# Kernel optimization log

Measured on AMD Instinct MI355X. Metric: run time of the kernel, lower is better.

Reference implementation:

```python
import jax, jax.numpy as jnp
import numpy as np

D = 128
N = 20000
E = 60000
L = 5  # levels 0..4; level 0 = primary inputs
PER = N // L
# processing order in the original forward: AND(3), NOT(2), XOR(5), MAJ(1), OR(4)
CODES = [3, 2, 5, 1, 4]
FIDX = {3: 0, 5: 1, 1: 2, 4: 3}  # index into 2D-input func aggregators


def _gru(x, h, wih, whh, bih, bhh):
    # single-step torch.nn.GRU cell. wih:[D,3D], whh:[D,3D]
    gi = x @ wih + bih
    gh = h @ whh + bhh
    ir, iz, inn = jnp.split(gi, 3, axis=-1)
    hr, hz, hn = jnp.split(gh, 3, axis=-1)
    r = jax.nn.sigmoid(ir + hr)
    z = jax.nn.sigmoid(iz + hz)
    n = jnp.tanh(inn + r * hn)
    return (1.0 - z) * n + z * h


def setup_inputs() -> dict:
    rng = np.random.default_rng(0)
    # topological levels, contiguous blocks of PER nodes per level
    forward_level = np.repeat(np.arange(L), PER).astype(np.int32)
    gate = np.zeros(N, dtype=np.int32)
    gate[PER:] = rng.integers(1, 6, size=N - PER)  # gates 1..5 for non-PI nodes
    # DAG edges: dst at level>=1, src strictly below dst's level
    dst = rng.integers(PER, N, size=E)
    dst_level = forward_level[dst].astype(np.int64)
    src = (rng.random(E) * (dst_level * PER)).astype(np.int64)
    edge_index = np.stack([src, dst]).astype(np.int32)

    key = jax.random.key(0)
    ks = iter(jax.random.split(key, 64))
    s = 0.08
    p = {}
    p['hs_init'] = jax.random.normal(next(ks), (N, D), jnp.float32)
    # strc aggregators (5 gate types, input D): 2-layer MLP
    p['Ws1'] = jax.random.normal(next(ks), (5, D, D)) * s
    p['bs1'] = jnp.zeros((5, D))
    p['Ws2'] = jax.random.normal(next(ks), (5, D, D)) * s
    p['bs2'] = jnp.zeros((5, D))
    # func aggregators with 2D input (and, xor, maj, or)
    p['Wf1'] = jax.random.normal(next(ks), (4, 2 * D, D)) * s
    p['bf1'] = jnp.zeros((4, D))
    p['Wf2'] = jax.random.normal(next(ks), (4, D, D)) * s
    p['bf2'] = jnp.zeros((4, D))
    # not_func aggregator (input D)
    p['Wnf1'] = jax.random.normal(next(ks), (D, D)) * s
    p['bnf1'] = jnp.zeros((D,))
    p['Wnf2'] = jax.random.normal(next(ks), (D, D)) * s
    p['bnf2'] = jnp.zeros((D,))
    # GRU params, stacked over 5 gate types, strc and func
    for pre in ('Gs', 'Gf'):
        p[pre + '_wih'] = jax.random.normal(next(ks), (5, D, 3 * D)) * s
        p[pre + '_whh'] = jax.random.normal(next(ks), (5, D, 3 * D)) * s
        p[pre + '_bih'] = jnp.zeros((5, 3 * D))
        p[pre + '_bhh'] = jnp.zeros((5, 3 * D))
    p['edge_index'] = jnp.asarray(edge_index)
    p['gate'] = jnp.asarray(gate)
    p['forward_level'] = jnp.asarray(forward_level)
    p['num_levels'] = L
    return p


def reference(hs_init, Ws1, bs1, Ws2, bs2, Wf1, bf1, Wf2, bf2,
              Wnf1, bnf1, Wnf2, bnf2,
              Gs_wih, Gs_whh, Gs_bih, Gs_bhh,
              Gf_wih, Gf_whh, Gf_bih, Gf_bhh,
              edge_index, gate, forward_level, num_levels):
    src, dst = edge_index[0], edge_index[1]
    pi_mask = (gate == 0)
    hs = jnp.where(pi_mask[:, None], hs_init, 0.0)  # generate_hs_init: encode PIs
    hf = jnp.zeros_like(hs)
    node_state = jnp.concatenate([hs, hf], axis=-1)

    for level in range(1, num_levels):
        for t, code in enumerate(CODES):
            nmask = (forward_level == level) & (gate == code)  # [N]
            emask = nmask[dst].astype(hs.dtype)[:, None]       # edges into these nodes
            # --- structural message: MLP(hs[src]) summed into dst
            m = jax.nn.relu(hs[src] @ Ws1[t] + bs1[t]) @ Ws2[t] + bs2[t]
            agg = jax.ops.segment_sum(m * emask, dst, num_segments=N)
            h_new = _gru(agg, hs, Gs_wih[t], Gs_whh[t], Gs_bih[t], Gs_bhh[t])
            hs = jnp.where(nmask[:, None], h_new, hs)
            # --- functional message
            if code == 2:  # NOT uses current hf only
                m = jax.nn.relu(hf[src] @ Wnf1 + bnf1) @ Wnf2 + bnf2
            else:
                fi = FIDX[code]
                m = jax.nn.relu(node_state[src] @ Wf1[fi] + bf1[fi]) @ Wf2[fi] + bf2[fi]
            agg = jax.ops.segment_sum(m * emask, dst, num_segments=N)
            h_new = _gru(agg, hf, Gf_wih[t], Gf_whh[t], Gf_bih[t], Gf_bhh[t])
            hf = jnp.where(nmask[:, None], h_new, hf)
        node_state = jnp.concatenate([hs, hf], axis=-1)
    return hs, hf
```

## Files before the change

kernel.cpp:

```cpp
#include <hip/hip_runtime.h>
#include <hip/hip_bf16.h>

typedef __hip_bfloat16 bf16;
typedef unsigned short ushortT;
typedef __attribute__((ext_vector_type(8))) short bf16x8;
typedef __attribute__((ext_vector_type(4))) float f32x4;

#define D 128
#define NLEV 5
#define TE 16
#define TN 16

#define OFF_S1 0
#define OFF_S2 81920
#define OFF_F1 163840
#define OFF_F2 294912
#define OFF_NF1 360448
#define OFF_NF2 376832
#define OFF_GSH 393216
#define OFF_GFH 638976
#define OFF_GSL 884736
#define OFF_GFL 1130496
#define WT_TOTAL 1376256

__constant__ int TMAP[6] = { -1, 3, 1, 0, 4, 2 };
__constant__ int FMAP[6] = { -1, 2, -1, 0, 3, 1 };

__device__ int g_flag;

__device__ __forceinline__ float sigm(float x) { return 1.0f / (1.0f + __expf(-x)); }

__device__ __forceinline__ ushortT f2b(float v) {
    bf16 h = __float2bfloat16(v);
    return *reinterpret_cast<ushortT*>(&h);
}

template <int ISB>
__device__ __forceinline__ float ld(const void* p, size_t i) {
    if (ISB) return __bfloat162float(((const bf16*)p)[i]);
    return ((const float*)p)[i];
}

__device__ __forceinline__ float ldx(int isb, const void* p, size_t i) {
    return isb ? __bfloat162float(((const bf16*)p)[i]) : ((const float*)p)[i];
}

__global__ __launch_bounds__(256) void setup_a(
    const void* __restrict__ hs_init, const int* __restrict__ gate,
    const int* __restrict__ dstA, const int* __restrict__ lev,
    int E, int N, int ND,
    ushortT* __restrict__ hsb, ushortT* __restrict__ hfb, void* __restrict__ out,
    float* __restrict__ agg_s, float* __restrict__ agg_f,
    int* __restrict__ ecnt, int* __restrict__ ncnt, int* __restrict__ ndeg,
    const void* Ws1, const void* Ws2, const void* Wf1, const void* Wf2,
    const void* Wnf1, const void* Wnf2, const void* Gs, const void* Gf,
    ushortT* __restrict__ wt, int B_init, int B_cnt) {
    __shared__ int sfl;
    __shared__ int lc[40];
    int tid = threadIdx.x;
    int bid = blockIdx.x;

    if (tid < 64) {
        float x = __bfloat162float(((const bf16*)hs_init)[2 * tid]);
        float ax = fabsf(x);
        bool sane = (x == 0.0f) || (ax > 1e-4f && ax < 64.0f);
        unsigned long long m = __ballot(sane);
        if (tid == 0) sfl = (__popcll(m) >= 32) ? 1 : 0;
    }
    __syncthreads();
    int isb = sfl;
    if (bid == 0 && tid == 0) g_flag = isb;

    if (bid < B_init) {
        int v = (bid << 1) | (tid >> 7);
        int j = tid & 127;
        if (v < N) {
            size_t idx = (size_t)v * D + j;
            bool pi = (gate[v] == 0);
            if (isb) {
                ushortT bval = pi ? ((const ushortT*)hs_init)[idx] : 0;
                hsb[idx] = bval; hfb[idx] = 0;
                ((ushortT*)out)[idx] = bval;
                ((ushortT*)out)[ND + idx] = 0;
            } else {
                float val = pi ? ((const float*)hs_init)[idx] : 0.f;
                hsb[idx] = f2b(val); hfb[idx] = 0;
                ((float*)out)[idx] = val;
                ((float*)out)[ND + idx] = 0.f;
            }
            agg_s[idx] = 0.f;
            agg_f[idx] = 0.f;
        }
    } else if (bid < B_init + B_cnt) {
        if (tid < 40) lc[tid] = 0;
        __syncthreads();
        int i = (bid - B_init) * 256 + tid;
        if (i < E) {
            int d = dstA[i]; int l = lev[d];
            if (l >= 1 && l < NLEV) {
                atomicAdd(&lc[(l - 1) * 5 + TMAP[gate[d]]], 1);
                atomicAdd(&ndeg[d], 1);
            }
        }
        if (i < N) {
            int l = lev[i];
            if (l >= 1 && l < NLEV && gate[i] >= 1)
                atomicAdd(&lc[20 + (l - 1) * 5 + TMAP[gate[i]]], 1);
        }
        __syncthreads();
        if (tid < 20 && lc[tid]) atomicAdd(&ecnt[tid], lc[tid]);
        if (tid >= 20 && tid < 40 && lc[tid]) atomicAdd(&ncnt[tid - 20], lc[tid]);
    } else {
        int i = (bid - B_init - B_cnt) * 256 + tid;
        if (i >= WT_TOTAL) return;
        const void* src; int Kd, C, rem, mode = 0;
        if (i < OFF_S2)       { src = Ws1;  rem = i;           Kd = 128; C = 128; }
        else if (i < OFF_F1)  { src = Ws2;  rem = i - OFF_S2;  Kd = 128; C = 128; }
        else if (i < OFF_F2)  { src = Wf1;  rem = i - OFF_F1;  Kd = 256; C = 128; }
        else if (i < OFF_NF1) { src = Wf2;  rem = i - OFF_F2;  Kd = 128; C = 128; }
        else if (i < OFF_NF2) { src = Wnf1; rem = i - OFF_NF1; Kd = 128; C = 128; }
        else if (i < OFF_GSH) { src = Wnf2; rem = i - OFF_NF2; Kd = 128; C = 128; }
        else if (i < OFF_GFH) { src = Gs;   rem = i - OFF_GSH; Kd = 128; C = 384; mode = 1; }
        else if (i < OFF_GSL) { src = Gf;   rem = i - OFF_GFH; Kd = 128; C = 384; mode = 1; }
        else if (i < OFF_GFL) { src = Gs;   rem = i - OFF_GSL; Kd = 128; C = 384; mode = 2; }
        else                  { src = Gf;   rem = i - OFF_GFL; Kd = 128; C = 384; mode = 2; }
        int n = rem / (Kd * C);
        int r2 = rem % (Kd * C);
        int c = r2 / Kd;
        int k = r2 % Kd;
        size_t si = (size_t)n * Kd * C + (size_t)k * C + c;
        float v = ldx(isb, src, si);
        ushortT o;
        if (mode == 2) {
            bf16 h = __float2bfloat16(v);
            o = f2b(v - __bfloat162float(h));
        } else {
            o = f2b(v);
        }
        wt[i] = o;
    }
}

__global__ void scan_offsets(const int* __restrict__ ecnt, const int* __restrict__ ncnt,
                             int* __restrict__ eoff, int* __restrict__ noff) {
    if (threadIdx.x == 0 && blockIdx.x == 0) {
        int o = 0;
        for (int b = 0; b < 20; ++b) { eoff[b] = o; o += ((ecnt[b] + TE - 1) / TE) * TE; }
        eoff[20] = o;
        o = 0;
        for (int b = 0; b < 20; ++b) { noff[b] = o; o += ((ncnt[b] + TN - 1) / TN) * TN; }
        noff[20] = o;
    }
}

__global__ void fill_bins(const int* __restrict__ gate, const int* __restrict__ lev, int N,
                          const int* __restrict__ noff, int* __restrict__ ncur,
                          int* __restrict__ nlist) {
    __shared__ int nc[20], nb[20];
    int tid = threadIdx.x;
    if (tid < 20) nc[tid] = 0;
    __syncthreads();
    int i = blockIdx.x * blockDim.x + tid;
    int bn = -1, rn = 0;
    if (i < N) {
        int l = lev[i];
        if (l >= 1 && l < NLEV && gate[i] >= 1) { bn = (l - 1) * 5 + TMAP[gate[i]]; rn = atomicAdd(&nc[bn], 1); }
    }
    __syncthreads();
    if (tid < 20) nb[tid] = nc[tid] ? atomicAdd(&ncur[tid], nc[tid]) : 0;
    __syncthreads();
    if (bn >= 0) nlist[noff[bn] + nb[bn] + rn] = i;
}

__global__ __launch_bounds__(256) void bucket_scan(
    const int* __restrict__ nlist, const int* __restrict__ noff,
    const int* __restrict__ ncnt, const int* __restrict__ eoff,
    const int* __restrict__ ndeg, int* __restrict__ nodeoff) {
    int b = blockIdx.x;
    int start = noff[b];
    int cnt = ncnt[b];
    int ebase = eoff[b];
    __shared__ int sc[256];
    int tid = threadIdx.x;
    int carry = 0;
    for (int chunk = 0; chunk < cnt; chunk += 256) {
        __syncthreads();
        int i = chunk + tid;
        int v = -1, dg = 0;
        if (i < cnt) { v = nlist[start + i]; dg = ndeg[v]; }
        sc[tid] = dg;
        __syncthreads();
        for (int off = 1; off < 256; off <<= 1) {
            int y = (tid >= off) ? sc[tid - off] : 0;
            __syncthreads();
            sc[tid] += y;
            __syncthreads();
        }
        if (v >= 0) nodeoff[v] = ebase + carry + (sc[tid] - dg);
        carry += sc[255];
    }
}

__global__ void fill_edges(const int* __restrict__ dstA, const int* __restrict__ lev,
                           int E, const int* __restrict__ nodeoff,
                           int* __restrict__ ecur_n, int* __restrict__ elist) {
    int i = blockIdx.x * blockDim.x + threadIdx.x;
    if (i >= E) return;
    int d = dstA[i];
    int l = lev[d];
    if (l >= 1 && l < NLEV) {
        int pos = nodeoff[d] + atomicAdd(&ecur_n[d], 1);
        elist[pos] = i;
    }
}

__global__ __launch_bounds__(256) void edge_mfma(
    const ushortT* __restrict__ hsb, const ushortT* __restrict__ hfb,
    const ushortT* __restrict__ wt,
    const void* __restrict__ bs1, const void* __restrict__ bs2,
    const void* __restrict__ bf1, const void* __restrict__ bf2,
    const void* __restrict__ bnf1, const void* __restrict__ bnf2,
    const int* __restrict__ dstA, const int* __restrict__ srcA,
    const int* __restrict__ gate,
    const int* __restrict__ eoff, const int* __restrict__ ecnt,
    const int* __restrict__ elist,
    float* __restrict__ agg_s, float* __restrict__ agg_f, int level) {
    int lvl = (level - 1) * 5;
    int lo = eoff[lvl];
    int hi = eoff[lvl + 5];
    int base = lo + blockIdx.x * TE;
    if (base >= hi) return;
    int b = 0;
#pragma unroll
    for (int bb = 1; bb < 5; ++bb) if (base >= eoff[lvl + bb]) b = bb;
    int nvalid = eoff[lvl + b] + ecnt[lvl + b] - base;
    if (nvalid <= 0) return;
    if (nvalid > TE) nvalid = TE;

    __shared__ int se[TE], de[TE];
    __shared__ bf16 hid[2][16][136];
    __shared__ float emsg[2][16][128];

    int tid = threadIdx.x;
    int wv = tid >> 6, pass = wv >> 1, hc = wv & 1, l = tid & 63;
    int lg = l >> 4, lr = l & 15;
    int isb = g_flag;

    int c = gate[dstA[elist[base]]];
    int t = TMAP[c], fi = FMAP[c];

    if (tid < TE) {
        if (tid < nvalid) {
            int e = elist[base + tid];
            se[tid] = srcA[e];
            de[tid] = dstA[e];
        } else {
            se[tid] = -1;
            de[tid] = -1;
        }
    }
    __syncthreads();

    int src = se[lr];

    int KS1; size_t wb1; int K1;
    if (pass == 0)      { KS1 = 4; wb1 = OFF_S1 + (size_t)t * 16384; K1 = 128; }
    else if (c == 2)    { KS1 = 4; wb1 = OFF_NF1; K1 = 128; }
    else                { KS1 = 8; wb1 = OFF_F1 + (size_t)fi * 32768; K1 = 256; }

    f32x4 a0 = {0.f,0.f,0.f,0.f}, a1 = a0, a2 = a0, a3 = a0;
    for (int ks = 0; ks < KS1; ++ks) {
        bf16x8 a = {0,0,0,0,0,0,0,0};
        if (src >= 0) {
            int kk = ks * 32 + lg * 8;
            const ushortT* ap;
            if (pass == 0)      ap = hsb + (size_t)src * D + kk;
            else if (c == 2)    ap = hfb + (size_t)src * D + kk;
            else                ap = (kk < 128) ? (hsb + (size_t)src * D + kk)
                                                : (hfb + (size_t)src * D + (kk - 128));
            a = *(const bf16x8*)ap;
        }
        int kb = ks * 32 + lg * 8;
        {
            bf16x8 b2 = *(const bf16x8*)&wt[wb1 + (size_t)(hc * 64 + 0 * 16 + lr) * K1 + kb];
            a0 = __builtin_amdgcn_mfma_f32_16x16x32_bf16(a, b2, a0, 0, 0, 0);
        }
        {
            bf16x8 b2 = *(const bf16x8*)&wt[wb1 + (size_t)(hc * 64 + 1 * 16 + lr) * K1 + kb];
            a1 = __builtin_amdgcn_mfma_f32_16x16x32_bf16(a, b2, a1, 0, 0, 0);
        }
        {
            bf16x8 b2 = *(const bf16x8*)&wt[wb1 + (size_t)(hc * 64 + 2 * 16 + lr) * K1 + kb];
            a2 = __builtin_amdgcn_mfma_f32_16x16x32_bf16(a, b2, a2, 0, 0, 0);
        }
        {
            bf16x8 b2 = *(const bf16x8*)&wt[wb1 + (size_t)(hc * 64 + 3 * 16 + lr) * K1 + kb];
            a3 = __builtin_amdgcn_mfma_f32_16x16x32_bf16(a, b2, a3, 0, 0, 0);
        }
    }

    const void* b1p = (pass == 0) ? bs1 : (c == 2 ? bnf1 : bf1);
    size_t b1o = (pass == 0) ? (size_t)t * D : (c == 2 ? 0 : (size_t)fi * D);
    {
        f32x4 av[4] = { a0, a1, a2, a3 };
#pragma unroll
        for (int ct = 0; ct < 4; ++ct) {
            int cc = hc * 64 + ct * 16 + lr;
            float bb = ldx(isb, b1p, b1o + cc);
#pragma unroll
            for (int r = 0; r < 4; ++r) {
                int m = lg * 4 + r;
                float v = fmaxf(av[ct][r] + bb, 0.f);
                hid[pass][m][cc] = __float2bfloat16(v);
            }
        }
    }
    __syncthreads();

    size_t wb2 = (pass == 0) ? (OFF_S2 + (size_t)t * 16384)
                             : (c == 2 ? (size_t)OFF_NF2 : (OFF_F2 + (size_t)fi * 16384));
    a0 = (f32x4){0.f,0.f,0.f,0.f}; a1 = a0; a2 = a0; a3 = a0;
#pragma unroll
    for (int ks = 0; ks < 4; ++ks) {
        bf16x8 a = *(const bf16x8*)&hid[pass][lr][ks * 32 + lg * 8];
        int kb = ks * 32 + lg * 8;
        {
            bf16x8 b2 = *(const bf16x8*)&wt[wb2 + (size_t)(hc * 64 + 0 * 16 + lr) * 128 + kb];
            a0 = __builtin_amdgcn_mfma_f32_16x16x32_bf16(a, b2, a0, 0, 0, 0);
        }
        {
            bf16x8 b2 = *(const bf16x8*)&wt[wb2 + (size_t)(hc * 64 + 1 * 16 + lr) * 128 + kb];
            a1 = __builtin_amdgcn_mfma_f32_16x16x32_bf16(a, b2, a1, 0, 0, 0);
        }
        {
            bf16x8 b2 = *(const bf16x8*)&wt[wb2 + (size_t)(hc * 64 + 2 * 16 + lr) * 128 + kb];
            a2 = __builtin_amdgcn_mfma_f32_16x16x32_bf16(a, b2, a2, 0, 0, 0);
        }
        {
            bf16x8 b2 = *(const bf16x8*)&wt[wb2 + (size_t)(hc * 64 + 3 * 16 + lr) * 128 + kb];
            a3 = __builtin_amdgcn_mfma_f32_16x16x32_bf16(a, b2, a3, 0, 0, 0);
        }
    }

    const void* b2p = (pass == 0) ? bs2 : (c == 2 ? bnf2 : bf2);
    size_t b2o = (pass == 0) ? (size_t)t * D : (c == 2 ? 0 : (size_t)fi * D);
    {
        f32x4 av[4] = { a0, a1, a2, a3 };
#pragma unroll
        for (int ct = 0; ct < 4; ++ct) {
            int cc = hc * 64 + ct * 16 + lr;
            float bb = ldx(isb, b2p, b2o + cc);
#pragma unroll
            for (int r = 0; r < 4; ++r) {
                int m = lg * 4 + r;
                emsg[pass][m][cc] = av[ct][r] + bb;
            }
        }
    }
    __syncthreads();

    float* aggp = pass ? agg_f : agg_s;
    int col = hc * 64 + l;
    float s = 0.f;
    for (int m = 0; m < TE; ++m) {
        int d = de[m];
        if (d < 0) break;
        s += emsg[pass][m][col];
        bool flush = (m == TE - 1) || (de[m + 1] != d);
        if (flush) {
            atomicAdd(&aggp[(size_t)d * D + col], s);
            s = 0.f;
        }
    }
}

template <int ISB>
__device__ void node_fused_body(
    const float* __restrict__ agg_s, const float* __restrict__ agg_f,
    const ushortT* __restrict__ wt,
    const void* __restrict__ Gs_bih, const void* __restrict__ Gs_bhh,
    const void* __restrict__ Gf_bih, const void* __restrict__ Gf_bhh,
    ushortT* __restrict__ hsb, ushortT* __restrict__ hfb,
    void* __restrict__ out, int ND,
    const int* __restrict__ gate,
    const int* __restrict__ noff, const int* __restrict__ ncnt,
    const int* __restrict__ nlist,
    int level, float (*gi)[3][16][128]) {
    int lvl = (level - 1) * 5;
    int lo = noff[lvl];
    int hi = noff[lvl + 5];
    int base = lo + blockIdx.x * TN;
    if (base >= hi) return;
    int b = 0;
#pragma unroll
    for (int bb = 1; bb < 5; ++bb) if (base >= noff[lvl + bb]) b = bb;
    int nvalid = noff[lvl + b] + ncnt[lvl + b] - base;
    if (nvalid <= 0) return;
    if (nvalid > TN) nvalid = TN;

    int tid = threadIdx.x;
    int w = tid >> 6, l = tid & 63;
    int lg = l >> 4, lr = l & 15;
    int p = w / 6, cg = w % 6;
    int t = TMAP[gate[nlist[base]]];

    const float* agg = p ? agg_f : agg_s;
    size_t wbh = (p ? OFF_GFH : OFF_GSH) + (size_t)t * 49152;
    size_t wbl = (p ? OFF_GFL : OFF_GSL) + (size_t)t * 49152;

    int v = (lr < nvalid) ? nlist[base + lr] : -1;

    f32x4 acc[4];
#pragma unroll
    for (int q = 0; q < 4; ++q) acc[q] = (f32x4){0.f, 0.f, 0.f, 0.f};

    for (int ks = 0; ks < 4; ++ks) {
        bf16x8 ahi = {0,0,0,0,0,0,0,0}, alo = ahi;
        if (v >= 0) {
            const float* ap = agg + (size_t)v * D + ks * 32 + lg * 8;
            float4 f0 = *(const float4*)ap;
            float4 f1 = *(const float4*)(ap + 4);
            float av[8] = { f0.x, f0.y, f0.z, f0.w, f1.x, f1.y, f1.z, f1.w };
#pragma unroll
            for (int j = 0; j < 8; ++j) {
                bf16 h = __float2bfloat16(av[j]);
                ahi[j] = (short)*reinterpret_cast<ushortT*>(&h);
                float r = av[j] - __bfloat162float(h);
                bf16 l2 = __float2bfloat16(r);
                alo[j] = (short)*reinterpret_cast<ushortT*>(&l2);
            }
        }
        int kb = ks * 32 + lg * 8;
#pragma unroll
        for (int q = 0; q < 4; ++q) {
            int col = (cg * 4 + q) * 16 + lr;
            bf16x8 bh = *(const bf16x8*)&wt[wbh + (size_t)col * 128 + kb];
            acc[q] = __builtin_amdgcn_mfma_f32_16x16x32_bf16(ahi, bh, acc[q], 0, 0, 0);
            acc[q] = __builtin_amdgcn_mfma_f32_16x16x32_bf16(alo, bh, acc[q], 0, 0, 0);
            if (!ISB) {
                bf16x8 bl = *(const bf16x8*)&wt[wbl + (size_t)col * 128 + kb];
                acc[q] = __builtin_amdgcn_mfma_f32_16x16x32_bf16(ahi, bl, acc[q], 0, 0, 0);
            }
        }
    }

#pragma unroll
    for (int q = 0; q < 4; ++q) {
        int ct = cg * 4 + q;
        int g = ct >> 3, j = (ct & 7) * 16 + lr;
#pragma unroll
        for (int r = 0; r < 4; ++r) gi[p][g][lg * 4 + r][j] = acc[q][r];
    }
    __syncthreads();

    if (tid < 256) {
        int pp = tid >> 7, j = tid & 127;
        const void* bih = pp ? Gf_bih : Gs_bih;
        const void* bhh = pp ? Gf_bhh : Gs_bhh;
        float br = ld<ISB>(bih, (size_t)t * 384 + j);
        float bz = ld<ISB>(bih, (size_t)t * 384 + 128 + j);
        float bn = ld<ISB>(bih, (size_t)t * 384 + 256 + j);
        float hr = ld<ISB>(bhh, (size_t)t * 384 + j);
        float hz = ld<ISB>(bhh, (size_t)t * 384 + 128 + j);
        float hn = ld<ISB>(bhh, (size_t)t * 384 + 256 + j);
        ushortT* hb = pp ? hfb : hsb;
#pragma unroll
        for (int r = 0; r < TN; ++r) {
            if (r >= nvalid) break;
            int vv = nlist[base + r];
            float rr = sigm(gi[pp][0][r][j] + br + hr);
            float z = sigm(gi[pp][1][r][j] + bz + hz);
            float n = tanhf(gi[pp][2][r][j] + bn + rr * hn);
            float outv = (1.f - z) * n;
            size_t oidx = (size_t)pp * ND + (size_t)vv * D + j;
            if (ISB) ((ushortT*)out)[oidx] = f2b(outv);
            else     ((float*)out)[oidx] = outv;
            hb[(size_t)vv * D + j] = f2b(outv);
        }
    }
}

__global__ __launch_bounds__(768) void node_fused(
    const float* agg_s, const float* agg_f, const ushortT* wt,
    const void* Gs_bih, const void* Gs_bhh,
    const void* Gf_bih, const void* Gf_bhh,
    ushortT* hsb, ushortT* hfb, void* out, int ND,
    const int* gate, const int* noff, const int* ncnt, const int* nlist, int level) {
    __shared__ float gi[2][3][16][128];
    if (g_flag)
        node_fused_body<1>(agg_s, agg_f, wt, Gs_bih, Gs_bhh, Gf_bih, Gf_bhh,
                           hsb, hfb, out, ND, gate, noff, ncnt, nlist, level, gi);
    else
        node_fused_body<0>(agg_s, agg_f, wt, Gs_bih, Gs_bhh, Gf_bih, Gf_bhh,
                           hsb, hfb, out, ND, gate, noff, ncnt, nlist, level, gi);
}

extern "C" void kernel_launch(void* const* d_in, const int* in_sizes, int n_in,
                              void* d_out, int out_size, void* d_ws, size_t ws_size,
                              hipStream_t stream) {
    const void* hs_init = d_in[0];
    const void* Ws1 = d_in[1];
    const void* bs1 = d_in[2];
    const void* Ws2 = d_in[3];
    const void* bs2 = d_in[4];
    const void* Wf1 = d_in[5];
    const void* bf1 = d_in[6];
    const void* Wf2 = d_in[7];
    const void* bf2 = d_in[8];
    const void* Wnf1 = d_in[9];
    const void* bnf1 = d_in[10];
    const void* Wnf2 = d_in[11];
    const void* bnf2 = d_in[12];
    const void* Gs_wih = d_in[13];
    const void* Gs_bih = d_in[15];
    const void* Gs_bhh = d_in[16];
    const void* Gf_wih = d_in[17];
    const void* Gf_bih = d_in[19];
    const void* Gf_bhh = d_in[20];
    const int* edge_index = (const int*)d_in[21];
    const int* gate = (const int*)d_in[22];
    const int* lev = (const int*)d_in[23];

    int E = in_sizes[21] / 2;
    int N = in_sizes[22];
    int ND = N * D;
    int cap = ((N / NLEV + 5 * TN + 64) + TN - 1) / TN * TN;

    float* agg_s = (float*)d_ws;
    float* agg_f = agg_s + ND;
    ushortT* hsb = (ushortT*)(agg_f + ND);
    ushortT* hfb = hsb + ND;
    ushortT* wt = hfb + ND;
    int* meta = (int*)(wt + WT_TOTAL);
    int* ecnt = meta;
    int* ncnt = ecnt + 20;
    int* ncur = ncnt + 20;
    int* eoff = ncur + 20;
    int* noff = eoff + 21;
    int* ndeg = meta + 128;
    int* ecur_n = ndeg + N;
    int* nodeoff = ecur_n + N;
    int* elist = nodeoff + N;
    int* nlist = elist + (E + 20 * TE);

    const int* srcA = edge_index;
    const int* dstA = edge_index + E;

    hipMemsetAsync(meta, 0, (size_t)(128 + 2 * N) * sizeof(int), stream);

    int mx = (E > N) ? E : N;
    int B_init = (N + 1) / 2;
    int B_cnt = (mx + 255) / 256;
    int B_prep = (WT_TOTAL + 255) / 256;
    setup_a<<<B_init + B_cnt + B_prep, 256, 0, stream>>>(
        hs_init, gate, dstA, lev, E, N, ND,
        hsb, hfb, d_out, agg_s, agg_f,
        ecnt, ncnt, ndeg,
        Ws1, Ws2, Wf1, Wf2, Wnf1, Wnf2, Gs_wih, Gf_wih,
        wt, B_init, B_cnt);

    scan_offsets<<<1, 64, 0, stream>>>(ecnt, ncnt, eoff, noff);
    fill_bins<<<(N + 255) / 256, 256, 0, stream>>>(gate, lev, N, noff, ncur, nlist);
    bucket_scan<<<20, 256, 0, stream>>>(nlist, noff, ncnt, eoff, ndeg, nodeoff);
    fill_edges<<<(E + 255) / 256, 256, 0, stream>>>(dstA, lev, E, nodeoff, ecur_n, elist);

    int gridE = (E + 20 * TE) / TE + 1;
    int gridNcap = cap / TN;
    for (int level = 1; level < NLEV; ++level) {
        edge_mfma<<<gridE, 256, 0, stream>>>(hsb, hfb, wt,
                                             bs1, bs2, bf1, bf2, bnf1, bnf2,
                                             dstA, srcA, gate, eoff, ecnt, elist,
                                             agg_s, agg_f, level);
        node_fused<<<gridNcap, 768, 0, stream>>>(agg_s, agg_f, wt,
                                                 Gs_bih, Gs_bhh, Gf_bih, Gf_bhh,
                                                 hsb, hfb, d_out, ND,
                                                 gate, noff, ncnt, nlist, level);
    }
}
```

Before: 242.1 us.

## Merge setup kernels, vectorize init, and make edge kernel grid-stride persistent

Folds the single-thread offset scan into every fill_bins block and merges fill_edges into the bucket scan kernel, which now has each of 20 blocks scan all edges for its own bucket. This cuts two kernel launches. The init path now writes 4 elements per thread with vector stores. edge_mfma changes from one launch-sized grid to a fixed 2048-block grid-stride loop to cut block launch overhead and reuse LDS, at the cost of extra block-level syncs per tile and 20x redundant edge reads in finish_buckets.

```diff
diff --git a/kernel.cpp b/kernel.cpp
--- a/kernel.cpp
+++ b/kernel.cpp
@@ -3,6 +3,7 @@
 
 typedef __hip_bfloat16 bf16;
 typedef unsigned short ushortT;
+typedef unsigned int uintT;
 typedef __attribute__((ext_vector_type(8))) short bf16x8;
 typedef __attribute__((ext_vector_type(4))) float f32x4;
 
@@ -10,6 +11,7 @@
 #define NLEV 5
 #define TE 16
 #define TN 16
+#define EGRID 2048
 
 #define OFF_S1 0
 #define OFF_S2 81920
@@ -72,24 +74,30 @@
     if (bid == 0 && tid == 0) g_flag = isb;
 
     if (bid < B_init) {
-        int v = (bid << 1) | (tid >> 7);
-        int j = tid & 127;
+        int v = (bid << 3) | (tid >> 5);
+        int j = (tid & 31) * 4;
         if (v < N) {
             size_t idx = (size_t)v * D + j;
             bool pi = (gate[v] == 0);
             if (isb) {
-                ushortT bval = pi ? ((const ushortT*)hs_init)[idx] : 0;
-                hsb[idx] = bval; hfb[idx] = 0;
-                ((ushortT*)out)[idx] = bval;
-                ((ushortT*)out)[ND + idx] = 0;
+                uint2 bv = make_uint2(0u, 0u);
+                if (pi) bv = *(const uint2*)((const ushortT*)hs_init + idx);
+                *(uint2*)&hsb[idx] = bv;
+                *(uint2*)&hfb[idx] = make_uint2(0u, 0u);
+                *(uint2*)&((ushortT*)out)[idx] = bv;
+                *(uint2*)&((ushortT*)out)[ND + idx] = make_uint2(0u, 0u);
             } else {
-                float val = pi ? ((const float*)hs_init)[idx] : 0.f;
-                hsb[idx] = f2b(val); hfb[idx] = 0;
-                ((float*)out)[idx] = val;
-                ((float*)out)[ND + idx] = 0.f;
-            }
-            agg_s[idx] = 0.f;
-            agg_f[idx] = 0.f;
+                float4 fv = make_float4(0.f, 0.f, 0.f, 0.f);
+                if (pi) fv = *(const float4*)((const float*)hs_init + idx);
+                ushortT b0 = f2b(fv.x), b1 = f2b(fv.y), b2 = f2b(fv.z), b3 = f2b(fv.w);
+                *(uint2*)&hsb[idx] = make_uint2((uintT)b0 | ((uintT)b1 << 16),
+                                                (uintT)b2 | ((uintT)b3 << 16));
+                *(uint2*)&hfb[idx] = make_uint2(0u, 0u);
+                *(float4*)&((float*)out)[idx] = fv;
+                *(float4*)&((float*)out)[ND + idx] = make_float4(0.f, 0.f, 0.f, 0.f);
+            }
+            *(float4*)&agg_s[idx] = make_float4(0.f, 0.f, 0.f, 0.f);
+            *(float4*)&agg_f[idx] = make_float4(0.f, 0.f, 0.f, 0.f);
         }
     } else if (bid < B_init + B_cnt) {
         if (tid < 40) lc[tid] = 0;
@@ -141,25 +149,27 @@
     }
 }
 
-__global__ void scan_offsets(const int* __restrict__ ecnt, const int* __restrict__ ncnt,
-                             int* __restrict__ eoff, int* __restrict__ noff) {
-    if (threadIdx.x == 0 && blockIdx.x == 0) {
-        int o = 0;
-        for (int b = 0; b < 20; ++b) { eoff[b] = o; o += ((ecnt[b] + TE - 1) / TE) * TE; }
-        eoff[20] = o;
-        o = 0;
-        for (int b = 0; b < 20; ++b) { noff[b] = o; o += ((ncnt[b] + TN - 1) / TN) * TN; }
-        noff[20] = o;
-    }
-}
-
 __global__ void fill_bins(const int* __restrict__ gate, const int* __restrict__ lev, int N,
-                          const int* __restrict__ noff, int* __restrict__ ncur,
-                          int* __restrict__ nlist) {
+                          const int* __restrict__ ecnt, const int* __restrict__ ncnt,
+                          int* __restrict__ eoff, int* __restrict__ noff,
+                          int* __restrict__ ncur, int* __restrict__ nlist) {
+    __shared__ int s_noff[21], s_eoff[21];
     __shared__ int nc[20], nb[20];
     int tid = threadIdx.x;
+    if (tid == 0) {
+        int o = 0;
+        for (int b = 0; b < 20; ++b) { s_noff[b] = o; o += ((ncnt[b] + TN - 1) / TN) * TN; }
+        s_noff[20] = o;
+        o = 0;
+        for (int b = 0; b < 20; ++b) { s_eoff[b] = o; o += ((ecnt[b] + TE - 1) / TE) * TE; }
+        s_eoff[20] = o;
+    }
     if (tid < 20) nc[tid] = 0;
     __syncthreads();
+    if (blockIdx.x == 0 && tid < 21) {
+        noff[tid] = s_noff[tid];
+        eoff[tid] = s_eoff[tid];
+    }
     int i = blockIdx.x * blockDim.x + tid;
     int bn = -1, rn = 0;
     if (i < N) {
@@ -169,13 +179,16 @@
     __syncthreads();
     if (tid < 20) nb[tid] = nc[tid] ? atomicAdd(&ncur[tid], nc[tid]) : 0;
     __syncthreads();
-    if (bn >= 0) nlist[noff[bn] + nb[bn] + rn] = i;
-}
-
-__global__ __launch_bounds__(256) void bucket_scan(
+    if (bn >= 0) nlist[s_noff[bn] + nb[bn] + rn] = i;
+}
+
+__global__ __launch_bounds__(256) void finish_buckets(
     const int* __restrict__ nlist, const int* __restrict__ noff,
     const int* __restrict__ ncnt, const int* __restrict__ eoff,
-    const int* __restrict__ ndeg, int* __restrict__ nodeoff) {
+    const int* __restrict__ ndeg, int* __restrict__ nodeoff,
+    const int* __restrict__ dstA, const int* __restrict__ lev,
+    const int* __restrict__ gate, int E,
+    int* __restrict__ ecur_n, int* __restrict__ elist) {
     int b = blockIdx.x;
     int start = noff[b];
     int cnt = ncnt[b];
@@ -199,16 +212,13 @@
         if (v >= 0) nodeoff[v] = ebase + carry + (sc[tid] - dg);
         carry += sc[255];
     }
-}
-
-__global__ void fill_edges(const int* __restrict__ dstA, const int* __restrict__ lev,
-                           int E, const int* __restrict__ nodeoff,
-                           int* __restrict__ ecur_n, int* __restrict__ elist) {
-    int i = blockIdx.x * blockDim.x + threadIdx.x;
-    if (i >= E) return;
-    int d = dstA[i];
-    int l = lev[d];
-    if (l >= 1 && l < NLEV) {
+    __threadfence_block();
+    __syncthreads();
+    int blev = b / 5 + 1, bt = b % 5;
+    for (int i = tid; i < E; i += 256) {
+        int d = dstA[i];
+        if (lev[d] != blev) continue;
+        if (TMAP[gate[d]] != bt) continue;
         int pos = nodeoff[d] + atomicAdd(&ecur_n[d], 1);
         elist[pos] = i;
     }
@@ -227,15 +237,7 @@
     float* __restrict__ agg_s, float* __restrict__ agg_f, int level) {
     int lvl = (level - 1) * 5;
     int lo = eoff[lvl];
-    int hi = eoff[lvl + 5];
-    int base = lo + blockIdx.x * TE;
-    if (base >= hi) return;
-    int b = 0;
-#pragma unroll
-    for (int bb = 1; bb < 5; ++bb) if (base >= eoff[lvl + bb]) b = bb;
-    int nvalid = eoff[lvl + b] + ecnt[lvl + b] - base;
-    if (nvalid <= 0) return;
-    if (nvalid > TE) nvalid = TE;
+    int nt = (eoff[lvl + 5] - lo) / TE;
 
     __shared__ int se[TE], de[TE];
     __shared__ bf16 hid[2][16][136];
@@ -246,131 +248,142 @@
     int lg = l >> 4, lr = l & 15;
     int isb = g_flag;
 
-    int c = gate[dstA[elist[base]]];
-    int t = TMAP[c], fi = FMAP[c];
-
-    if (tid < TE) {
-        if (tid < nvalid) {
-            int e = elist[base + tid];
-            se[tid] = srcA[e];
-            de[tid] = dstA[e];
-        } else {
-            se[tid] = -1;
-            de[tid] = -1;
-        }
-    }
-    __syncthreads();
-
-    int src = se[lr];
-
-    int KS1; size_t wb1; int K1;
-    if (pass == 0)      { KS1 = 4; wb1 = OFF_S1 + (size_t)t * 16384; K1 = 128; }
-    else if (c == 2)    { KS1 = 4; wb1 = OFF_NF1; K1 = 128; }
-    else                { KS1 = 8; wb1 = OFF_F1 + (size_t)fi * 32768; K1 = 256; }
-
-    f32x4 a0 = {0.f,0.f,0.f,0.f}, a1 = a0, a2 = a0, a3 = a0;
-    for (int ks = 0; ks < KS1; ++ks) {
-        bf16x8 a = {0,0,0,0,0,0,0,0};
-        if (src >= 0) {
-            int kk = ks * 32 + lg * 8;
-            const ushortT* ap;
-            if (pass == 0)      ap = hsb + (size_t)src * D + kk;
-            else if (c == 2)    ap = hfb + (size_t)src * D + kk;
-            else                ap = (kk < 128) ? (hsb + (size_t)src * D + kk)
-                                                : (hfb + (size_t)src * D + (kk - 128));
-            a = *(const bf16x8*)ap;
-        }
-        int kb = ks * 32 + lg * 8;
+    for (int ti = blockIdx.x; ti < nt; ti += gridDim.x) {
+        int base = lo + ti * TE;
+        int b = 0;
+#pragma unroll
+        for (int bb = 1; bb < 5; ++bb) if (base >= eoff[lvl + bb]) b = bb;
+        int nvalid = eoff[lvl + b] + ecnt[lvl + b] - base;
+        if (nvalid <= 0) continue;
+        if (nvalid > TE) nvalid = TE;
+
+        int c = gate[dstA[elist[base]]];
+        int t = TMAP[c], fi = FMAP[c];
+
+        if (tid < TE) {
+            if (tid < nvalid) {
+                int e = elist[base + tid];
+                se[tid] = srcA[e];
+                de[tid] = dstA[e];
+            } else {
+                se[tid] = -1;
+                de[tid] = -1;
+            }
+        }
+        __syncthreads();
+
+        int src = se[lr];
+
+        int KS1; size_t wb1; int K1;
+        if (pass == 0)      { KS1 = 4; wb1 = OFF_S1 + (size_t)t * 16384; K1 = 128; }
+        else if (c == 2)    { KS1 = 4; wb1 = OFF_NF1; K1 = 128; }
+        else                { KS1 = 8; wb1 = OFF_F1 + (size_t)fi * 32768; K1 = 256; }
+
+        f32x4 a0 = {0.f,0.f,0.f,0.f}, a1 = a0, a2 = a0, a3 = a0;
+        for (int ks = 0; ks < KS1; ++ks) {
+            bf16x8 a = {0,0,0,0,0,0,0,0};
+            if (src >= 0) {
+                int kk = ks * 32 + lg * 8;
+                const ushortT* ap;
+                if (pass == 0)      ap = hsb + (size_t)src * D + kk;
+                else if (c == 2)    ap = hfb + (size_t)src * D + kk;
+                else                ap = (kk < 128) ? (hsb + (size_t)src * D + kk)
+                                                    : (hfb + (size_t)src * D + (kk - 128));
+                a = *(const bf16x8*)ap;
+            }
+            int kb = ks * 32 + lg * 8;
+            {
+                bf16x8 b2 = *(const bf16x8*)&wt[wb1 + (size_t)(hc * 64 + 0 * 16 + lr) * K1 + kb];
+                a0 = __builtin_amdgcn_mfma_f32_16x16x32_bf16(a, b2, a0, 0, 0, 0);
+            }
+            {
+                bf16x8 b2 = *(const bf16x8*)&wt[wb1 + (size_t)(hc * 64 + 1 * 16 + lr) * K1 + kb];
+                a1 = __builtin_amdgcn_mfma_f32_16x16x32_bf16(a, b2, a1, 0, 0, 0);
+            }
+            {
+                bf16x8 b2 = *(const bf16x8*)&wt[wb1 + (size_t)(hc * 64 + 2 * 16 + lr) * K1 + kb];
+                a2 = __builtin_amdgcn_mfma_f32_16x16x32_bf16(a, b2, a2, 0, 0, 0);
+            }
+            {
+                bf16x8 b2 = *(const bf16x8*)&wt[wb1 + (size_t)(hc * 64 + 3 * 16 + lr) * K1 + kb];
+                a3 = __builtin_amdgcn_mfma_f32_16x16x32_bf16(a, b2, a3, 0, 0, 0);
+            }
+        }
+
+        const void* b1p = (pass == 0) ? bs1 : (c == 2 ? bnf1 : bf1);
+        size_t b1o = (pass == 0) ? (size_t)t * D : (c == 2 ? 0 : (size_t)fi * D);
         {
-            bf16x8 b2 = *(const bf16x8*)&wt[wb1 + (size_t)(hc * 64 + 0 * 16 + lr) * K1 + kb];
-            a0 = __builtin_amdgcn_mfma_f32_16x16x32_bf16(a, b2, a0, 0, 0, 0);
-        }
+            f32x4 av[4] = { a0, a1, a2, a3 };
+#pragma unroll
+            for (int ct = 0; ct < 4; ++ct) {
+                int cc = hc * 64 + ct * 16 + lr;
+                float bb = ldx(isb, b1p, b1o + cc);
+#pragma unroll
+                for (int r = 0; r < 4; ++r) {
+                    int m = lg * 4 + r;
+                    float v = fmaxf(av[ct][r] + bb, 0.f);
+                    hid[pass][m][cc] = __float2bfloat16(v);
+                }
+            }
+        }
+        __syncthreads();
+
+        size_t wb2 = (pass == 0) ? (OFF_S2 + (size_t)t * 16384)
+                                 : (c == 2 ? (size_t)OFF_NF2 : (OFF_F2 + (size_t)fi * 16384));
+        a0 = (f32x4){0.f,0.f,0.f,0.f}; a1 = a0; a2 = a0; a3 = a0;
+#pragma unroll
+        for (int ks = 0; ks < 4; ++ks) {
+            bf16x8 a = *(const bf16x8*)&hid[pass][lr][ks * 32 + lg * 8];
+            int kb = ks * 32 + lg * 8;
+            {
+                bf16x8 b2 = *(const bf16x8*)&wt[wb2 + (size_t)(hc * 64 + 0 * 16 + lr) * 128 + kb];
+                a0 = __builtin_amdgcn_mfma_f32_16x16x32_bf16(a, b2, a0, 0, 0, 0);
+            }
+            {
+                bf16x8 b2 = *(const bf16x8*)&wt[wb2 + (size_t)(hc * 64 + 1 * 16 + lr) * 128 + kb];
+                a1 = __builtin_amdgcn_mfma_f32_16x16x32_bf16(a, b2, a1, 0, 0, 0);
+            }
+            {
+                bf16x8 b2 = *(const bf16x8*)&wt[wb2 + (size_t)(hc * 64 + 2 * 16 + lr) * 128 + kb];
+                a2 = __builtin_amdgcn_mfma_f32_16x16x32_bf16(a, b2, a2, 0, 0, 0);
+            }
+            {
+                bf16x8 b2 = *(const bf16x8*)&wt[wb2 + (size_t)(hc * 64 + 3 * 16 + lr) * 128 + kb];
+                a3 = __builtin_amdgcn_mfma_f32_16x16x32_bf16(a, b2, a3, 0, 0, 0);
+            }
+        }
+
+        const void* b2p = (pass == 0) ? bs2 : (c == 2 ? bnf2 : bf2);
+        size_t b2o = (pass == 0) ? (size_t)t * D : (c == 2 ? 0 : (size_t)fi * D);
         {
-            bf16x8 b2 = *(const bf16x8*)&wt[wb1 + (size_t)(hc * 64 + 1 * 16 + lr) * K1 + kb];
-            a1 = __builtin_amdgcn_mfma_f32_16x16x32_bf16(a, b2, a1, 0, 0, 0);
-        }
-        {
-            bf16x8 b2 = *(const bf16x8*)&wt[wb1 + (size_t)(hc * 64 + 2 * 16 + lr) * K1 + kb];
-            a2 = __builtin_amdgcn_mfma_f32_16x16x32_bf16(a, b2, a2, 0, 0, 0);
-        }
-        {
-            bf16x8 b2 = *(const bf16x8*)&wt[wb1 + (size_t)(hc * 64 + 3 * 16 + lr) * K1 + kb];
-            a3 = __builtin_amdgcn_mfma_f32_16x16x32_bf16(a, b2, a3, 0, 0, 0);
-        }
-    }
-
-    const void* b1p = (pass == 0) ? bs1 : (c == 2 ? bnf1 : bf1);
-    size_t b1o = (pass == 0) ? (size_t)t * D : (c == 2 ? 0 : (size_t)fi * D);
-    {
-        f32x4 av[4] = { a0, a1, a2, a3 };
-#pragma unroll
-        for (int ct = 0; ct < 4; ++ct) {
-            int cc = hc * 64 + ct * 16 + lr;
-            float bb = ldx(isb, b1p, b1o + cc);
-#pragma unroll
-            for (int r = 0; r < 4; ++r) {
-                int m = lg * 4 + r;
-                float v = fmaxf(av[ct][r] + bb, 0.f);
-                hid[pass][m][cc] = __float2bfloat16(v);
-            }
-        }
-    }
-    __syncthreads();
-
-    size_t wb2 = (pass == 0) ? (OFF_S2 + (size_t)t * 16384)
-                             : (c == 2 ? (size_t)OFF_NF2 : (OFF_F2 + (size_t)fi * 16384));
-    a0 = (f32x4){0.f,0.f,0.f,0.f}; a1 = a0; a2 = a0; a3 = a0;
-#pragma unroll
-    for (int ks = 0; ks < 4; ++ks) {
-        bf16x8 a = *(const bf16x8*)&hid[pass][lr][ks * 32 + lg * 8];
-        int kb = ks * 32 + lg * 8;
-        {
-            bf16x8 b2 = *(const bf16x8*)&wt[wb2 + (size_t)(hc * 64 + 0 * 16 + lr) * 128 + kb];
-            a0 = __builtin_amdgcn_mfma_f32_16x16x32_bf16(a, b2, a0, 0, 0, 0);
-        }
-        {
-            bf16x8 b2 = *(const bf16x8*)&wt[wb2 + (size_t)(hc * 64 + 1 * 16 + lr) * 128 + kb];
-            a1 = __builtin_amdgcn_mfma_f32_16x16x32_bf16(a, b2, a1, 0, 0, 0);
-        }
-        {
-            bf16x8 b2 = *(const bf16x8*)&wt[wb2 + (size_t)(hc * 64 + 2 * 16 + lr) * 128 + kb];
-            a2 = __builtin_amdgcn_mfma_f32_16x16x32_bf16(a, b2, a2, 0, 0, 0);
-        }
-        {
-            bf16x8 b2 = *(const bf16x8*)&wt[wb2 + (size_t)(hc * 64 + 3 * 16 + lr) * 128 + kb];
-            a3 = __builtin_amdgcn_mfma_f32_16x16x32_bf16(a, b2, a3, 0, 0, 0);
-        }
-    }
-
-    const void* b2p = (pass == 0) ? bs2 : (c == 2 ? bnf2 : bf2);
-    size_t b2o = (pass == 0) ? (size_t)t * D : (c == 2 ? 0 : (size_t)fi * D);
-    {
-        f32x4 av[4] = { a0, a1, a2, a3 };
-#pragma unroll
-        for (int ct = 0; ct < 4; ++ct) {
-            int cc = hc * 64 + ct * 16 + lr;
-            float bb = ldx(isb, b2p, b2o + cc);
-#pragma unroll
-            for (int r = 0; r < 4; ++r) {
-                int m = lg * 4 + r;
-                emsg[pass][m][cc] = av[ct][r] + bb;
-            }
-        }
-    }
-    __syncthreads();
-
-    float* aggp = pass ? agg_f : agg_s;
-    int col = hc * 64 + l;
-    float s = 0.f;
-    for (int m = 0; m < TE; ++m) {
-        int d = de[m];
-        if (d < 0) break;
-        s += emsg[pass][m][col];
-        bool flush = (m == TE - 1) || (de[m + 1] != d);
-        if (flush) {
-            atomicAdd(&aggp[(size_t)d * D + col], s);
-            s = 0.f;
-        }
+            f32x4 av[4] = { a0, a1, a2, a3 };
+#pragma unroll
+            for (int ct = 0; ct < 4; ++ct) {
+                int cc = hc * 64 + ct * 16 + lr;
+                float bb = ldx(isb, b2p, b2o + cc);
+#pragma unroll
+                for (int r = 0; r < 4; ++r) {
+                    int m = lg * 4 + r;
+                    emsg[pass][m][cc] = av[ct][r] + bb;
+                }
+            }
+        }
+        __syncthreads();
+
+        float* aggp = pass ? agg_f : agg_s;
+        int col = hc * 64 + l;
+        float s = 0.f;
+        for (int m = 0; m < TE; ++m) {
+            int d = de[m];
+            if (d < 0) break;
+            s += emsg[pass][m][col];
+            bool flush = (m == TE - 1) || (de[m + 1] != d);
+            if (flush) {
+                atomicAdd(&aggp[(size_t)d * D + col], s);
+                s = 0.f;
+            }
+        }
+        __syncthreads();
     }
 }
 
@@ -549,7 +562,7 @@
     hipMemsetAsync(meta, 0, (size_t)(128 + 2 * N) * sizeof(int), stream);
 
     int mx = (E > N) ? E : N;
-    int B_init = (N + 1) / 2;
+    int B_init = (N + 7) / 8;
     int B_cnt = (mx + 255) / 256;
     int B_prep = (WT_TOTAL + 255) / 256;
     setup_a<<<B_init + B_cnt + B_prep, 256, 0, stream>>>(
@@ -559,15 +572,14 @@
         Ws1, Ws2, Wf1, Wf2, Wnf1, Wnf2, Gs_wih, Gf_wih,
         wt, B_init, B_cnt);
 
-    scan_offsets<<<1, 64, 0, stream>>>(ecnt, ncnt, eoff, noff);
-    fill_bins<<<(N + 255) / 256, 256, 0, stream>>>(gate, lev, N, noff, ncur, nlist);
-    bucket_scan<<<20, 256, 0, stream>>>(nlist, noff, ncnt, eoff, ndeg, nodeoff);
-    fill_edges<<<(E + 255) / 256, 256, 0, stream>>>(dstA, lev, E, nodeoff, ecur_n, elist);
-
-    int gridE = (E + 20 * TE) / TE + 1;
+    fill_bins<<<(N + 255) / 256, 256, 0, stream>>>(gate, lev, N, ecnt, ncnt,
+                                                   eoff, noff, ncur, nlist);
+    finish_buckets<<<20, 256, 0, stream>>>(nlist, noff, ncnt, eoff, ndeg, nodeoff,
+                                           dstA, lev, gate, E, ecur_n, elist);
+
     int gridNcap = cap / TN;
     for (int level = 1; level < NLEV; ++level) {
-        edge_mfma<<<gridE, 256, 0, stream>>>(hsb, hfb, wt,
+        edge_mfma<<<EGRID, 256, 0, stream>>>(hsb, hfb, wt,
                                              bs1, bs2, bf1, bf2, bnf1, bnf2,
                                              dstA, srcA, gate, eoff, ecnt, elist,
                                              agg_s, agg_f, level);
```

New measurement: 493.3 us. 104% more time.
